# Performance work log

Hardware: AMD Instinct MI355X
Metric: run time of the kernel (lower is better)

Reference implementation:

```python
import jax, jax.numpy as jnp
import numpy as np

S, B, H, K, P = 512, 64, 8, 12, 9        # seq_len, input_bits, num_heads, bits_per_neuron, position bits
L = 2 * B + P                            # head input bits = 137
T = 2 ** K                               # RAM table entries per neuron = 4096
THRESH = H // 2                          # majority-vote threshold


def setup_inputs() -> dict:
    key = jax.random.key(0)
    k1, k2, k3 = jax.random.split(key, 3)
    tokens = jax.random.randint(k1, (S, B), 0, 2, dtype=jnp.int32)           # bit tokens
    conn = jax.random.randint(k2, (H, B, K), 0, L, dtype=jnp.int32)          # random neuron connections
    ram = jnp.round(jax.random.uniform(k3, (H, B, T), dtype=jnp.float32))    # binary RAM contents
    return {"tokens": tokens, "conn": conn, "ram": ram}


def _partial_addr(bits, idx, mask, w):
    # bits: [M, nbits] int; idx/mask: [H,B,K]; w: [K]. Returns [H,B,M] partial RAM address.
    g = bits[:, idx]                                           # [M,H,B,K]
    contrib = jnp.sum(g * (mask.astype(jnp.int32) * w), axis=-1)  # [M,H,B]
    return jnp.moveaxis(contrib, 0, -1)                        # [H,B,M]


def reference(tokens, conn, ram):
    w = (2 ** jnp.arange(K)).astype(jnp.int32)                 # bit weight per connection slot
    # Each connection reads from concat(query_bits[B], key_bits[B], rel_pos_bits[P]).
    is_q = conn < B
    is_k = (conn >= B) & (conn < 2 * B)
    is_r = conn >= 2 * B
    qi = jnp.where(is_q, conn, 0)
    ki = jnp.where(is_k, conn - B, 0)
    ri = jnp.where(is_r, conn - 2 * B, 0)
    d = jnp.arange(S)
    relbits = ((d[:, None] >> jnp.arange(P)) & 1).astype(jnp.int32)  # [S,P] binary rel distance
    # RAM address decomposes additively over the three bit sources.
    Aq = _partial_addr(tokens, qi, is_q, w)                    # [H,B,S] query part (per i)
    Ak = _partial_addr(tokens, ki, is_k, w)                    # [H,B,S] key part (per j)
    Ar = _partial_addr(relbits, ri, is_r, w)                   # [H,B,S] rel-dist part (per i-j)
    dij = jnp.maximum(d[:, None] - d[None, :], 0)              # [S,S] causal rel distance
    addr = Aq[:, :, :, None] + Ak[:, :, None, :] + Ar[:, :, dij]  # [H,B,S,S]
    val = jnp.take_along_axis(ram, addr.reshape(H, B, S * S), axis=2).reshape(H, B, S, S)
    mask = jnp.tril(jnp.ones((S, S), dtype=val.dtype))         # causal: only j <= i contribute
    parity = jnp.mod(jnp.sum(val * mask, axis=-1), 2.0)        # XOR accumulation over keys -> [H,B,S]
    votes = jnp.sum(parity, axis=0)                            # [B,S] ones-count across heads
    out = (votes > THRESH).astype(jnp.float32).T               # [S,B] bit-majority vote
    return out
```

## Files before the change

kernel.cpp:

```cpp
#include <hip/hip_runtime.h>
#include <stdint.h>

#define WS_TABLE  0
#define WS_TOKROW 65536
#define WS_PAR    66560

__global__ __launch_bounds__(256) void softram_pack_kernel(
    const int* __restrict__ tokens,
    const float* __restrict__ ram,
    uint32_t* __restrict__ ws)
{
    const int tid = threadIdx.x, lane = tid & 63, w = tid >> 6;
    if (blockIdx.x < 512) {
        const int hb = blockIdx.x;
        const float* ramp = ram + (size_t)hb * 4096;
        uint32_t* tp = ws + WS_TABLE + hb * 128;
        #pragma unroll
        for (int c = 0; c < 16; ++c) {
            float v = ramp[c * 256 + tid];
            unsigned long long m = __ballot(v > 0.5f);
            if (lane == 0) {
                tp[c * 8 + w * 2]     = (uint32_t)m;
                tp[c * 8 + w * 2 + 1] = (uint32_t)(m >> 32);
            }
        }
    } else {
        const int r = blockIdx.x - 512;
        unsigned long long* tokp = (unsigned long long*)(ws + WS_TOKROW);
        for (int c = r * 16; c < r * 16 + 16; ++c) {
            int v = tokens[c * 256 + tid];
            unsigned long long m = __ballot(v != 0);
            if (lane == 0) tokp[c * 4 + w] = m;
        }
    }
}

__global__ __launch_bounds__(256) void softram_parity_kernel(
    const int* __restrict__ conn,
    uint32_t* __restrict__ ws)
{
    __shared__ uint32_t table[128];
    __shared__ unsigned long long tokrow[512];
    __shared__ unsigned short AqL[512], AkL[512], ArL[512];
    __shared__ unsigned long long parbuf[4];

    const int tid  = threadIdx.x;
    const int lane = tid & 63;
    const int w    = tid >> 6;
    const int hb   = blockIdx.x >> 2;
    const int q    = blockIdx.x & 3;

    if (tid < 128) table[tid] = ws[WS_TABLE + hb * 128 + tid];
    {
        const unsigned long long* tokp = (const unsigned long long*)(ws + WS_TOKROW);
        tokrow[tid]       = tokp[tid];
        tokrow[tid + 256] = tokp[tid + 256];
    }
    __syncthreads();

    const int* cp = conn + hb * 12;
    int ck[12];
    #pragma unroll
    for (int k = 0; k < 12; ++k) ck[k] = cp[k];
    #pragma unroll
    for (int rep = 0; rep < 2; ++rep) {
        int s = tid + rep * 256;
        unsigned long long row = tokrow[s];
        int aq = 0, ak = 0, ar = 0;
        #pragma unroll
        for (int k = 0; k < 12; ++k) {
            int c = ck[k];
            if (c < 64)       aq |= (int)((row >> c) & 1ull) << k;
            else if (c < 128) ak |= (int)((row >> (c - 64)) & 1ull) << k;
            else              ar |= ((s >> (c - 128)) & 1) << k;
        }
        AqL[s] = (unsigned short)aq;
        AkL[s] = (unsigned short)ak;
        ArL[s] = (unsigned short)ar;
    }
    __syncthreads();

    const int c  = (w < 2) ? q : (7 - q);
    const int hh = w & 1;
    const int i  = c * 64 + lane;
    const int aq = (int)AqL[i];
    uint32_t acc = 0;

    for (int sb = hh; sb < c; sb += 2) {
        int akv = (int)AkL[sb * 64 + lane];
        #pragma unroll
        for (int jj = 0; jj < 64; ++jj) {
            int sak = __builtin_amdgcn_readlane(akv, jj);
            int d = i - sb * 64 - jj;
            int addr = aq + sak + (int)ArL[d];
            acc ^= table[addr >> 5] >> (addr & 31);
        }
    }
    if (hh == (c & 1)) {
        int akv = (int)AkL[c * 64 + lane];
        #pragma unroll
        for (int jj = 0; jj < 64; ++jj) {
            int sak = __builtin_amdgcn_readlane(akv, jj);
            int d = lane - jj;
            int dm = d < 0 ? 0 : d;
            int addr = aq + sak + (int)ArL[dm];
            uint32_t bit = table[addr >> 5] >> (addr & 31);
            acc ^= (d >= 0) ? bit : 0u;
        }
    }
    acc &= 1u;
    unsigned long long m = __ballot(acc != 0);
    if (lane == 0) parbuf[w] = m;
    __syncthreads();

    if (tid == 0) {
        unsigned long long m0 = parbuf[0] ^ parbuf[1];
        unsigned long long m1 = parbuf[2] ^ parbuf[3];
        uint32_t* wp = ws + WS_PAR;
        wp[(hb * 8 + q) * 2]           = (uint32_t)m0;
        wp[(hb * 8 + q) * 2 + 1]       = (uint32_t)(m0 >> 32);
        wp[(hb * 8 + (7 - q)) * 2]     = (uint32_t)m1;
        wp[(hb * 8 + (7 - q)) * 2 + 1] = (uint32_t)(m1 >> 32);
    }
}

__global__ __launch_bounds__(256) void softram_vote_kernel(
    const uint32_t* __restrict__ ws, float* __restrict__ out)
{
    int t = blockIdx.x * 256 + threadIdx.x;
    int b = t & 63;
    int i = t >> 6;
    const uint32_t* wp = ws + WS_PAR;
    int sum = 0;
    #pragma unroll
    for (int h = 0; h < 8; ++h) {
        int hb = h * 64 + b;
        uint32_t wv = wp[(hb * 8 + (i >> 6)) * 2 + ((i >> 5) & 1)];
        sum += (wv >> (i & 31)) & 1u;
    }
    out[t] = (sum > 4) ? 1.0f : 0.0f;
}

extern "C" void kernel_launch(void* const* d_in, const int* in_sizes, int n_in,
                              void* d_out, int out_size, void* d_ws, size_t ws_size,
                              hipStream_t stream) {
    const int*   tokens = (const int*)d_in[0];
    const int*   conn   = (const int*)d_in[1];
    const float* ram    = (const float*)d_in[2];
    float*       out    = (float*)d_out;
    uint32_t*    ws     = (uint32_t*)d_ws;

    softram_pack_kernel<<<520, 256, 0, stream>>>(tokens, ram, ws);
    softram_parity_kernel<<<2048, 256, 0, stream>>>(conn, ws);
    softram_vote_kernel<<<128, 256, 0, stream>>>(ws, out);
}
```

Baseline: 104.4 us.

## Precompute Aq/Ak in pack kernel and specialize parity loop on relative-bit count

The pack kernel now computes the per-(head,bit) query and key partial addresses directly from tokens and writes them to workspace, so the parity blocks no longer rebuild them from packed token rows. The parity loop replaces the shared-memory ArL lookup with inline bit extraction from the relative distance, using templated variants for 0, 1 or 2 relative-position connections and a generic fallback for more. Work is redistributed so each wave handles both chunks with a stride-4 sweep over key blocks, which balances the triangular workload. The __noinline__ calls and the runtime switch add call overhead and register pressure, and the pack kernel grows to 1024 blocks of uncoalesced token reads.

```diff
diff --git a/kernel.cpp b/kernel.cpp
--- a/kernel.cpp
+++ b/kernel.cpp
@@ -1,12 +1,14 @@
 #include <hip/hip_runtime.h>
 #include <stdint.h>
 
-#define WS_TABLE  0
-#define WS_TOKROW 65536
-#define WS_PAR    66560
+#define WS_TABLE 0
+#define WS_AK    65536
+#define WS_AQ    196608
+#define WS_PAR   327680
 
 __global__ __launch_bounds__(256) void softram_pack_kernel(
     const int* __restrict__ tokens,
+    const int* __restrict__ conn,
     const float* __restrict__ ram,
     uint32_t* __restrict__ ws)
 {
@@ -25,24 +27,96 @@
             }
         }
     } else {
-        const int r = blockIdx.x - 512;
-        unsigned long long* tokp = (unsigned long long*)(ws + WS_TOKROW);
-        for (int c = r * 16; c < r * 16 + 16; ++c) {
-            int v = tokens[c * 256 + tid];
-            unsigned long long m = __ballot(v != 0);
-            if (lane == 0) tokp[c * 4 + w] = m;
-        }
-    }
+        const int hb = blockIdx.x - 512;
+        const int* cp = conn + hb * 12;
+        int ck[12];
+        #pragma unroll
+        for (int k = 0; k < 12; ++k) ck[k] = cp[k];
+        unsigned short* akg = (unsigned short*)(ws + WS_AK) + hb * 512;
+        unsigned short* aqg = (unsigned short*)(ws + WS_AQ) + hb * 512;
+        #pragma unroll
+        for (int rep = 0; rep < 2; ++rep) {
+            int s = tid + rep * 256;
+            int aq = 0, ak = 0;
+            #pragma unroll
+            for (int k = 0; k < 12; ++k) {
+                int c = ck[k];
+                if (c < 64)       aq |= tokens[s * 64 + c] << k;
+                else if (c < 128) ak |= tokens[s * 64 + (c - 64)] << k;
+            }
+            aqg[s] = (unsigned short)aq;
+            akg[s] = (unsigned short)ak;
+        }
+    }
+}
+
+template<int NR>
+__device__ __noinline__ uint32_t chunk_parity(
+    int c, int w, int lane, int aq,
+    const unsigned short* AkL, const uint32_t* tbl,
+    int p0, int k0, int p1, int k1)
+{
+    uint32_t acc = 0;
+    for (int sb = w; sb <= c; sb += 4) {
+        int akv = (int)AkL[sb * 64 + lane];
+        int dbase = (c - sb) * 64 + lane;
+        if (sb < c) {
+            #pragma unroll
+            for (int jj = 0; jj < 64; ++jj) {
+                int sak = __builtin_amdgcn_readlane(akv, jj);
+                int d = dbase - jj;
+                int addr = aq + sak;
+                if (NR > 0) addr += ((d >> p0) & 1) << k0;
+                if (NR > 1) addr += ((d >> p1) & 1) << k1;
+                acc ^= tbl[addr >> 5] >> (addr & 31);
+            }
+        } else {
+            #pragma unroll
+            for (int jj = 0; jj < 64; ++jj) {
+                int sak = __builtin_amdgcn_readlane(akv, jj);
+                int d = lane - jj;
+                int dm = d < 0 ? 0 : d;
+                int addr = aq + sak;
+                if (NR > 0) addr += ((dm >> p0) & 1) << k0;
+                if (NR > 1) addr += ((dm >> p1) & 1) << k1;
+                uint32_t bit = tbl[addr >> 5] >> (addr & 31);
+                acc ^= (d >= 0) ? bit : 0u;
+            }
+        }
+    }
+    return acc;
+}
+
+__device__ __noinline__ uint32_t chunk_parity_gen(
+    int c, int w, int lane, int aq,
+    const unsigned short* AkL, const uint32_t* tbl,
+    int nr, const int* rp, const int* rk)
+{
+    uint32_t acc = 0;
+    for (int sb = w; sb <= c; sb += 4) {
+        int akv = (int)AkL[sb * 64 + lane];
+        int dbase = (c - sb) * 64 + lane;
+        bool tail = (sb == c);
+        #pragma unroll 8
+        for (int jj = 0; jj < 64; ++jj) {
+            int sak = __builtin_amdgcn_readlane(akv, jj);
+            int d = dbase - jj;
+            int dm = d < 0 ? 0 : d;
+            int addr = aq + sak;
+            for (int t = 0; t < nr; ++t) addr += ((dm >> rp[t]) & 1) << rk[t];
+            uint32_t bit = tbl[addr >> 5] >> (addr & 31);
+            acc ^= (!tail || d >= 0) ? bit : 0u;
+        }
+    }
+    return acc;
 }
 
 __global__ __launch_bounds__(256) void softram_parity_kernel(
-    const int* __restrict__ conn,
-    uint32_t* __restrict__ ws)
-{
-    __shared__ uint32_t table[128];
-    __shared__ unsigned long long tokrow[512];
-    __shared__ unsigned short AqL[512], AkL[512], ArL[512];
-    __shared__ unsigned long long parbuf[4];
+    const int* __restrict__ conn, uint32_t* __restrict__ ws)
+{
+    __shared__ uint32_t tbl[128];
+    __shared__ unsigned short AkL[512];
+    __shared__ unsigned long long parbuf[2][4];
 
     const int tid  = threadIdx.x;
     const int lane = tid & 63;
@@ -50,77 +124,52 @@
     const int hb   = blockIdx.x >> 2;
     const int q    = blockIdx.x & 3;
 
-    if (tid < 128) table[tid] = ws[WS_TABLE + hb * 128 + tid];
-    {
-        const unsigned long long* tokp = (const unsigned long long*)(ws + WS_TOKROW);
-        tokrow[tid]       = tokp[tid];
-        tokrow[tid + 256] = tokp[tid + 256];
-    }
+    if (tid < 128) tbl[tid] = ws[WS_TABLE + hb * 128 + tid];
+    ((uint32_t*)AkL)[tid] = ws[WS_AK + hb * 256 + tid];
     __syncthreads();
 
     const int* cp = conn + hb * 12;
-    int ck[12];
+    int nr = 0, rp[12], rk[12];
     #pragma unroll
-    for (int k = 0; k < 12; ++k) ck[k] = cp[k];
+    for (int k = 0; k < 12; ++k) {
+        int cv = cp[k];
+        if (cv >= 128) { rp[nr] = cv - 128; rk[nr] = k; ++nr; }
+    }
+
+    const unsigned short* aqg = (const unsigned short*)(ws + WS_AQ) + hb * 512;
+    const int chunks[2] = { q, 7 - q };
+    uint32_t accs[2];
+
+    for (int ci = 0; ci < 2; ++ci) {
+        const int c  = chunks[ci];
+        const int aq = (int)aqg[c * 64 + lane];
+        uint32_t a;
+        switch (nr) {
+            case 0:  a = chunk_parity<0>(c, w, lane, aq, AkL, tbl, 0, 0, 0, 0); break;
+            case 1:  a = chunk_parity<1>(c, w, lane, aq, AkL, tbl, rp[0], rk[0], 0, 0); break;
+            case 2:  a = chunk_parity<2>(c, w, lane, aq, AkL, tbl, rp[0], rk[0], rp[1], rk[1]); break;
+            default: a = chunk_parity_gen(c, w, lane, aq, AkL, tbl, nr, rp, rk); break;
+        }
+        accs[ci] = a & 1u;
+    }
+
     #pragma unroll
-    for (int rep = 0; rep < 2; ++rep) {
-        int s = tid + rep * 256;
-        unsigned long long row = tokrow[s];
-        int aq = 0, ak = 0, ar = 0;
-        #pragma unroll
-        for (int k = 0; k < 12; ++k) {
-            int c = ck[k];
-            if (c < 64)       aq |= (int)((row >> c) & 1ull) << k;
-            else if (c < 128) ak |= (int)((row >> (c - 64)) & 1ull) << k;
-            else              ar |= ((s >> (c - 128)) & 1) << k;
-        }
-        AqL[s] = (unsigned short)aq;
-        AkL[s] = (unsigned short)ak;
-        ArL[s] = (unsigned short)ar;
+    for (int ci = 0; ci < 2; ++ci) {
+        unsigned long long m = __ballot(accs[ci] != 0);
+        if (lane == 0) parbuf[ci][w] = m;
     }
     __syncthreads();
 
-    const int c  = (w < 2) ? q : (7 - q);
-    const int hh = w & 1;
-    const int i  = c * 64 + lane;
-    const int aq = (int)AqL[i];
-    uint32_t acc = 0;
-
-    for (int sb = hh; sb < c; sb += 2) {
-        int akv = (int)AkL[sb * 64 + lane];
-        #pragma unroll
-        for (int jj = 0; jj < 64; ++jj) {
-            int sak = __builtin_amdgcn_readlane(akv, jj);
-            int d = i - sb * 64 - jj;
-            int addr = aq + sak + (int)ArL[d];
-            acc ^= table[addr >> 5] >> (addr & 31);
-        }
-    }
-    if (hh == (c & 1)) {
-        int akv = (int)AkL[c * 64 + lane];
-        #pragma unroll
-        for (int jj = 0; jj < 64; ++jj) {
-            int sak = __builtin_amdgcn_readlane(akv, jj);
-            int d = lane - jj;
-            int dm = d < 0 ? 0 : d;
-            int addr = aq + sak + (int)ArL[dm];
-            uint32_t bit = table[addr >> 5] >> (addr & 31);
-            acc ^= (d >= 0) ? bit : 0u;
-        }
-    }
-    acc &= 1u;
-    unsigned long long m = __ballot(acc != 0);
-    if (lane == 0) parbuf[w] = m;
-    __syncthreads();
-
     if (tid == 0) {
-        unsigned long long m0 = parbuf[0] ^ parbuf[1];
-        unsigned long long m1 = parbuf[2] ^ parbuf[3];
         uint32_t* wp = ws + WS_PAR;
-        wp[(hb * 8 + q) * 2]           = (uint32_t)m0;
-        wp[(hb * 8 + q) * 2 + 1]       = (uint32_t)(m0 >> 32);
-        wp[(hb * 8 + (7 - q)) * 2]     = (uint32_t)m1;
-        wp[(hb * 8 + (7 - q)) * 2 + 1] = (uint32_t)(m1 >> 32);
+        #pragma unroll
+        for (int ci = 0; ci < 2; ++ci) {
+            int c = chunks[ci];
+            unsigned long long m = parbuf[ci][0] ^ parbuf[ci][1]
+                                 ^ parbuf[ci][2] ^ parbuf[ci][3];
+            wp[(hb * 8 + c) * 2]     = (uint32_t)m;
+            wp[(hb * 8 + c) * 2 + 1] = (uint32_t)(m >> 32);
+        }
     }
 }
 
@@ -150,7 +199,7 @@
     float*       out    = (float*)d_out;
     uint32_t*    ws     = (uint32_t*)d_ws;
 
-    softram_pack_kernel<<<520, 256, 0, stream>>>(tokens, ram, ws);
+    softram_pack_kernel<<<1024, 256, 0, stream>>>(tokens, conn, ram, ws);
     softram_parity_kernel<<<2048, 256, 0, stream>>>(conn, ws);
     softram_vote_kernel<<<128, 256, 0, stream>>>(ws, out);
 }
```

Measured after the change: 153.1 us. +46.7%, slower.
